# Kernel tuning notes

Hardware: AMD Instinct MI355X
Metric: run time of the kernel (lower is better)

## Reference

```python
import jax, jax.numpy as jnp
import numpy as np

SCALE = 0.2  # scale init arg, clipped to [0,1]


def _relative_corners(rank):
    # [2**rank, rank] matrix of +-1 corner coordinates
    return jnp.array([[float(int(c)) * 2.0 - 1.0 for c in format(i, '0%db' % rank)]
                      for i in range(2 ** rank)], dtype=jnp.float32)


def _affine_from_noise(random_u):
    # random_u: [B, 2**r, r] uniform(0,1) -> random_scale uniform(1-SCALE, 1)
    B, n, r = random_u.shape
    out_c = _relative_corners(r)                                  # [2^r, r]
    random_scale = (1.0 - SCALE) + SCALE * random_u
    src = out_c[None] * random_scale                              # [B, 2^r, r]
    ones_col = jnp.ones((B, n, 1), jnp.float32)
    A = jnp.broadcast_to(
        jnp.concatenate([out_c, jnp.ones((n, 1), jnp.float32)], -1)[None],
        (B, n, r + 1))                                            # output corners (homog.)
    Bmat = jnp.concatenate([src, ones_col], -1)                   # source corners (homog.)
    # least-squares solve A X = B  (matrix_solve_ls): X = (A^T A)^{-1} A^T B
    AtA = jnp.einsum('bni,bnj->bij', A, A)
    AtB = jnp.einsum('bni,bnj->bij', A, Bmat)
    X = jnp.linalg.solve(AtA, AtB)                                # [B, r+1, r+1]
    return jnp.transpose(X, (0, 2, 1))                            # transform, [B, r+1, r+1]


def _make_grid(transform, spatial_shape):
    # AffineGridWarper: output voxel coords normalized to [-1,1], affine-mapped,
    # then converted to source pixel coordinates [0, size-1].
    r = len(spatial_shape)
    axes = [jnp.linspace(-1.0, 1.0, s) for s in spatial_shape]
    mesh = jnp.stack(jnp.meshgrid(*axes, indexing='ij'), -1)      # [D,H,W,r]
    mesh_h = jnp.concatenate(
        [mesh, jnp.ones(tuple(spatial_shape) + (1,), jnp.float32)], -1)
    coords = jnp.einsum('dhwj,bij->bdhwi', mesh_h, transform[:, :r, :])  # [B,D,H,W,r]
    sizes = jnp.array(spatial_shape, jnp.float32)
    return (coords + 1.0) * (sizes - 1.0) * 0.5                   # pixel coords


def _resample_linear_zero(img, coords):
    # trilinear interpolation with zero boundary: out-of-range corners contribute 0
    # img: [B,D,H,W,C], coords: [B,D,H,W,3] (pixel coordinates)
    B = img.shape[0]
    sp = jnp.array(img.shape[1:4], jnp.int32)
    f = jnp.floor(coords)
    frac = coords - f                                             # [B,D,H,W,3]
    i0 = f.astype(jnp.int32)
    bidx = jnp.arange(B)[:, None, None, None]
    out = jnp.zeros(img.shape, img.dtype)
    for corner in range(8):  # fixed structural loop over 2^3 interpolation corners
        off = jnp.array([(corner >> 2) & 1, (corner >> 1) & 1, corner & 1], jnp.int32)
        idx = i0 + off
        valid = jnp.all((idx >= 0) & (idx < sp), axis=-1)         # [B,D,H,W]
        ci = jnp.clip(idx, 0, sp - 1)
        vals = img[bidx, ci[..., 0], ci[..., 1], ci[..., 2]]      # [B,D,H,W,C]
        w = jnp.prod(jnp.where(off == 1, frac, 1.0 - frac), axis=-1)
        w = w * valid.astype(img.dtype)
        out = out + vals * w[..., None]
    return out


def setup_inputs() -> dict:
    key = jax.random.key(0)
    k1, k2 = jax.random.split(key)
    input_tensor = jax.random.normal(k1, (8, 128, 128, 128, 1), dtype=jnp.float32)
    random_u = jax.random.uniform(k2, (8, 8, 3), dtype=jnp.float32)
    return {"input_tensor": input_tensor, "random_u": random_u}


def reference(input_tensor, random_u):
    transform = _affine_from_noise(random_u)                      # [B,4,4]
    grid = _make_grid(transform, input_tensor.shape[1:4])         # [B,D,H,W,3]
    return _resample_linear_zero(input_tensor, grid)
```

## Files before the change

kernel.cpp:

```cpp
#include <hip/hip_runtime.h>

#define NB   8
#define NS   128
#define VOXELS_PER_B (NS*NS*NS)

__global__ void affine_from_noise_kernel(const float* __restrict__ u,
                                         float* __restrict__ T) {
    int b = threadIdx.x;
    if (b >= NB) return;
    float t[3][4];
#pragma unroll
    for (int i = 0; i < 3; ++i)
#pragma unroll
        for (int j = 0; j < 4; ++j) t[i][j] = 0.0f;

#pragma unroll
    for (int n = 0; n < 8; ++n) {
        float c0 = (n & 4) ? 1.0f : -1.0f;
        float c1 = (n & 2) ? 1.0f : -1.0f;
        float c2 = (n & 1) ? 1.0f : -1.0f;
        float c[3] = {c0, c1, c2};
#pragma unroll
        for (int i = 0; i < 3; ++i) {
            float s  = 0.8f + 0.2f * u[(b * 8 + n) * 3 + i];
            float bi = c[i] * s;
            t[i][0] += c[0] * bi;
            t[i][1] += c[1] * bi;
            t[i][2] += c[2] * bi;
            t[i][3] += bi;
        }
    }
#pragma unroll
    for (int i = 0; i < 3; ++i)
#pragma unroll
        for (int j = 0; j < 4; ++j)
            T[b * 12 + i * 4 + j] = t[i][j] * 0.125f;
}

__global__ __launch_bounds__(256) void warp_resample_kernel(
        const float* __restrict__ img, const float* __restrict__ T,
        float* __restrict__ out) {
    int gid   = blockIdx.x * 256 + threadIdx.x;
    int obase = gid << 2;
    int rem   = obase & (VOXELS_PER_B - 1);
    int d     = rem >> 14;
    int h     = (rem >> 7) & (NS - 1);
    int w     = rem & (NS - 1);

    __shared__ float t[12];
    int b = (int)((blockIdx.x * 1024u) >> 21);
    if (threadIdx.x < 12) t[threadIdx.x] = T[b * 12 + threadIdx.x];
    __syncthreads();

    const float inv = 2.0f / 127.0f;
    float x = -1.0f + d * inv;
    float y = -1.0f + h * inv;
    float z = -1.0f + w * inv;

    float q0 = (t[0] * x + t[1] * y + t[2]  * z + t[3]  + 1.0f) * 63.5f;
    float q1 = (t[4] * x + t[5] * y + t[6]  * z + t[7]  + 1.0f) * 63.5f;
    float q2 = (t[8] * x + t[9] * y + t[10] * z + t[11] + 1.0f) * 63.5f;
    float dp0 = t[2], dp1 = t[6], dp2 = t[10];

    const float* __restrict__ base = img + (size_t)b * VOXELS_PER_B;
    float res[4];

#pragma unroll
    for (int k = 0; k < 4; ++k) {
        float f0 = floorf(q0), f1 = floorf(q1), f2 = floorf(q2);
        int   i0 = (int)f0,    i1 = (int)f1,    i2 = (int)f2;
        float r0 = q0 - f0,    r1 = q1 - f1,    r2 = q2 - f2;

        bool ok = ((unsigned)i0 < 127u) && ((unsigned)i1 < 127u) &&
                  ((unsigned)i2 < 127u);
        float acc;
        if (__all(ok)) {
            const float* p = base + (((i0 << 7) + i1) << 7) + i2;
            float v000 = p[0],            v001 = p[1];
            float v010 = p[NS],           v011 = p[NS + 1];
            float v100 = p[NS * NS],      v101 = p[NS * NS + 1];
            float v110 = p[NS * NS + NS], v111 = p[NS * NS + NS + 1];
            float a0 = v000 + r2 * (v001 - v000);
            float a1 = v010 + r2 * (v011 - v010);
            float a2 = v100 + r2 * (v101 - v100);
            float a3 = v110 + r2 * (v111 - v110);
            float b0 = a0 + r1 * (a1 - a0);
            float b1 = a2 + r1 * (a3 - a2);
            acc = b0 + r0 * (b1 - b0);
        } else {
            float wd0 = (i0 >= 0     && i0 < NS)     ? (1.0f - r0) : 0.0f;
            float wd1 = (i0 + 1 >= 0 && i0 + 1 < NS) ? r0          : 0.0f;
            float wh0 = (i1 >= 0     && i1 < NS)     ? (1.0f - r1) : 0.0f;
            float wh1 = (i1 + 1 >= 0 && i1 + 1 < NS) ? r1          : 0.0f;
            float ww0 = (i2 >= 0     && i2 < NS)     ? (1.0f - r2) : 0.0f;
            float ww1 = (i2 + 1 >= 0 && i2 + 1 < NS) ? r2          : 0.0f;

            int cd0 = min(max(i0,     0), NS - 1);
            int cd1 = min(max(i0 + 1, 0), NS - 1);
            int ch0 = min(max(i1,     0), NS - 1);
            int ch1 = min(max(i1 + 1, 0), NS - 1);
            int cw0 = min(max(i2,     0), NS - 1);
            int cw1 = min(max(i2 + 1, 0), NS - 1);

            int r00 = (cd0 * NS + ch0) * NS;
            int r01 = (cd0 * NS + ch1) * NS;
            int r10 = (cd1 * NS + ch0) * NS;
            int r11 = (cd1 * NS + ch1) * NS;

            float v000 = base[r00 + cw0], v001 = base[r00 + cw1];
            float v010 = base[r01 + cw0], v011 = base[r01 + cw1];
            float v100 = base[r10 + cw0], v101 = base[r10 + cw1];
            float v110 = base[r11 + cw0], v111 = base[r11 + cw1];

            acc = v000 * (wd0 * wh0 * ww0)
                + v001 * (wd0 * wh0 * ww1)
                + v010 * (wd0 * wh1 * ww0)
                + v011 * (wd0 * wh1 * ww1)
                + v100 * (wd1 * wh0 * ww0)
                + v101 * (wd1 * wh0 * ww1)
                + v110 * (wd1 * wh1 * ww0)
                + v111 * (wd1 * wh1 * ww1);
        }
        res[k] = acc;
        q0 += dp0; q1 += dp1; q2 += dp2;
    }

    float4 o = make_float4(res[0], res[1], res[2], res[3]);
    *reinterpret_cast<float4*>(out + obase) = o;
}

extern "C" void kernel_launch(void* const* d_in, const int* in_sizes, int n_in,
                              void* d_out, int out_size, void* d_ws, size_t ws_size,
                              hipStream_t stream) {
    const float* img = (const float*)d_in[0];
    const float* u   = (const float*)d_in[1];
    float* out = (float*)d_out;
    float* T   = (float*)d_ws;

    affine_from_noise_kernel<<<1, 64, 0, stream>>>(u, T);

    int total   = NB * VOXELS_PER_B;
    int threads = total / 4;
    int blocks  = threads / 256;
    warp_resample_kernel<<<blocks, 256, 0, stream>>>(img, T, out);
}
```

Baseline: 146.1 us.

## Fuse transform setup into resample kernel and remap threads along depth

Removes the separate affine-setup kernel launch by having each block compute the 12 transform coefficients from the noise tensor in shared memory. Each thread now owns one (h,w) column and four consecutive depth slices rather than four consecutive w voxels, so lanes within a wavefront cover adjacent w and their gathers coalesce. The in-bounds test is hoisted so a single wave-wide __all decides between the fast and the clamped path for all four samples. In exchange the output writes become four scalar strided stores instead of one float4 store, and every block repeats the small transform computation.

```diff
diff --git a/kernel.cpp b/kernel.cpp
--- a/kernel.cpp
+++ b/kernel.cpp
@@ -4,103 +4,92 @@
 #define NS   128
 #define VOXELS_PER_B (NS*NS*NS)
 
-__global__ void affine_from_noise_kernel(const float* __restrict__ u,
-                                         float* __restrict__ T) {
-    int b = threadIdx.x;
-    if (b >= NB) return;
-    float t[3][4];
-#pragma unroll
-    for (int i = 0; i < 3; ++i)
-#pragma unroll
-        for (int j = 0; j < 4; ++j) t[i][j] = 0.0f;
-
-#pragma unroll
-    for (int n = 0; n < 8; ++n) {
-        float c0 = (n & 4) ? 1.0f : -1.0f;
-        float c1 = (n & 2) ? 1.0f : -1.0f;
-        float c2 = (n & 1) ? 1.0f : -1.0f;
-        float c[3] = {c0, c1, c2};
-#pragma unroll
-        for (int i = 0; i < 3; ++i) {
-            float s  = 0.8f + 0.2f * u[(b * 8 + n) * 3 + i];
-            float bi = c[i] * s;
-            t[i][0] += c[0] * bi;
-            t[i][1] += c[1] * bi;
-            t[i][2] += c[2] * bi;
-            t[i][3] += bi;
-        }
-    }
-#pragma unroll
-    for (int i = 0; i < 3; ++i)
-#pragma unroll
-        for (int j = 0; j < 4; ++j)
-            T[b * 12 + i * 4 + j] = t[i][j] * 0.125f;
-}
-
 __global__ __launch_bounds__(256) void warp_resample_kernel(
-        const float* __restrict__ img, const float* __restrict__ T,
+        const float* __restrict__ img, const float* __restrict__ u,
         float* __restrict__ out) {
-    int gid   = blockIdx.x * 256 + threadIdx.x;
-    int obase = gid << 2;
-    int rem   = obase & (VOXELS_PER_B - 1);
-    int d     = rem >> 14;
-    int h     = (rem >> 7) & (NS - 1);
-    int w     = rem & (NS - 1);
+    int tid = threadIdx.x;
+    int gid = blockIdx.x * 256 + tid;
+    int w    = gid & (NS - 1);
+    int h    = (gid >> 7) & (NS - 1);
+    int dblk = (gid >> 14) & 31;
+    int b    = blockIdx.x >> 11;
 
     __shared__ float t[12];
-    int b = (int)((blockIdx.x * 1024u) >> 21);
-    if (threadIdx.x < 12) t[threadIdx.x] = T[b * 12 + threadIdx.x];
+    if (tid < 12) {
+        int i = tid >> 2;
+        int j = tid & 3;
+        float acc = 0.0f;
+#pragma unroll
+        for (int n = 0; n < 8; ++n) {
+            float ci = (n & (4 >> i)) ? 1.0f : -1.0f;
+            float cj = (j < 3) ? ((n & (4 >> j)) ? 1.0f : -1.0f) : 1.0f;
+            float s  = 0.8f + 0.2f * u[(b * 8 + n) * 3 + i];
+            acc += cj * ci * s;
+        }
+        t[tid] = acc * 0.125f;
+    }
     __syncthreads();
 
     const float inv = 2.0f / 127.0f;
-    float x = -1.0f + d * inv;
-    float y = -1.0f + h * inv;
-    float z = -1.0f + w * inv;
+    int   d0 = dblk << 2;
+    float x  = -1.0f + d0 * inv;
+    float y  = -1.0f + h * inv;
+    float z  = -1.0f + w * inv;
 
     float q0 = (t[0] * x + t[1] * y + t[2]  * z + t[3]  + 1.0f) * 63.5f;
     float q1 = (t[4] * x + t[5] * y + t[6]  * z + t[7]  + 1.0f) * 63.5f;
     float q2 = (t[8] * x + t[9] * y + t[10] * z + t[11] + 1.0f) * 63.5f;
-    float dp0 = t[2], dp1 = t[6], dp2 = t[10];
+    float dq0 = t[0], dq1 = t[4], dq2 = t[8];
+
+    int   i0[4], i1[4], i2[4];
+    float r0[4], r1[4], r2[4];
+    bool  allok = true;
+#pragma unroll
+    for (int k = 0; k < 4; ++k) {
+        float f0 = floorf(q0), f1 = floorf(q1), f2 = floorf(q2);
+        i0[k] = (int)f0; i1[k] = (int)f1; i2[k] = (int)f2;
+        r0[k] = q0 - f0; r1[k] = q1 - f1; r2[k] = q2 - f2;
+        allok = allok && ((unsigned)i0[k] < 127u) &&
+                         ((unsigned)i1[k] < 127u) &&
+                         ((unsigned)i2[k] < 127u);
+        q0 += dq0; q1 += dq1; q2 += dq2;
+    }
 
     const float* __restrict__ base = img + (size_t)b * VOXELS_PER_B;
     float res[4];
 
+    if (__all(allok)) {
 #pragma unroll
-    for (int k = 0; k < 4; ++k) {
-        float f0 = floorf(q0), f1 = floorf(q1), f2 = floorf(q2);
-        int   i0 = (int)f0,    i1 = (int)f1,    i2 = (int)f2;
-        float r0 = q0 - f0,    r1 = q1 - f1,    r2 = q2 - f2;
-
-        bool ok = ((unsigned)i0 < 127u) && ((unsigned)i1 < 127u) &&
-                  ((unsigned)i2 < 127u);
-        float acc;
-        if (__all(ok)) {
-            const float* p = base + (((i0 << 7) + i1) << 7) + i2;
+        for (int k = 0; k < 4; ++k) {
+            const float* p = base + (((i0[k] << 7) + i1[k]) << 7) + i2[k];
             float v000 = p[0],            v001 = p[1];
             float v010 = p[NS],           v011 = p[NS + 1];
             float v100 = p[NS * NS],      v101 = p[NS * NS + 1];
             float v110 = p[NS * NS + NS], v111 = p[NS * NS + NS + 1];
-            float a0 = v000 + r2 * (v001 - v000);
-            float a1 = v010 + r2 * (v011 - v010);
-            float a2 = v100 + r2 * (v101 - v100);
-            float a3 = v110 + r2 * (v111 - v110);
-            float b0 = a0 + r1 * (a1 - a0);
-            float b1 = a2 + r1 * (a3 - a2);
-            acc = b0 + r0 * (b1 - b0);
-        } else {
-            float wd0 = (i0 >= 0     && i0 < NS)     ? (1.0f - r0) : 0.0f;
-            float wd1 = (i0 + 1 >= 0 && i0 + 1 < NS) ? r0          : 0.0f;
-            float wh0 = (i1 >= 0     && i1 < NS)     ? (1.0f - r1) : 0.0f;
-            float wh1 = (i1 + 1 >= 0 && i1 + 1 < NS) ? r1          : 0.0f;
-            float ww0 = (i2 >= 0     && i2 < NS)     ? (1.0f - r2) : 0.0f;
-            float ww1 = (i2 + 1 >= 0 && i2 + 1 < NS) ? r2          : 0.0f;
+            float a0 = v000 + r2[k] * (v001 - v000);
+            float a1 = v010 + r2[k] * (v011 - v010);
+            float a2 = v100 + r2[k] * (v101 - v100);
+            float a3 = v110 + r2[k] * (v111 - v110);
+            float b0 = a0 + r1[k] * (a1 - a0);
+            float b1 = a2 + r1[k] * (a3 - a2);
+            res[k] = b0 + r0[k] * (b1 - b0);
+        }
+    } else {
+#pragma unroll
+        for (int k = 0; k < 4; ++k) {
+            float wd0 = (i0[k] >= 0     && i0[k] < NS)     ? (1.0f - r0[k]) : 0.0f;
+            float wd1 = (i0[k] + 1 >= 0 && i0[k] + 1 < NS) ? r0[k]          : 0.0f;
+            float wh0 = (i1[k] >= 0     && i1[k] < NS)     ? (1.0f - r1[k]) : 0.0f;
+            float wh1 = (i1[k] + 1 >= 0 && i1[k] + 1 < NS) ? r1[k]          : 0.0f;
+            float ww0 = (i2[k] >= 0     && i2[k] < NS)     ? (1.0f - r2[k]) : 0.0f;
+            float ww1 = (i2[k] + 1 >= 0 && i2[k] + 1 < NS) ? r2[k]          : 0.0f;
 
-            int cd0 = min(max(i0,     0), NS - 1);
-            int cd1 = min(max(i0 + 1, 0), NS - 1);
-            int ch0 = min(max(i1,     0), NS - 1);
-            int ch1 = min(max(i1 + 1, 0), NS - 1);
-            int cw0 = min(max(i2,     0), NS - 1);
-            int cw1 = min(max(i2 + 1, 0), NS - 1);
+            int cd0 = min(max(i0[k],     0), NS - 1);
+            int cd1 = min(max(i0[k] + 1, 0), NS - 1);
+            int ch0 = min(max(i1[k],     0), NS - 1);
+            int ch1 = min(max(i1[k] + 1, 0), NS - 1);
+            int cw0 = min(max(i2[k],     0), NS - 1);
+            int cw1 = min(max(i2[k] + 1, 0), NS - 1);
 
             int r00 = (cd0 * NS + ch0) * NS;
             int r01 = (cd0 * NS + ch1) * NS;
@@ -112,21 +101,21 @@
             float v100 = base[r10 + cw0], v101 = base[r10 + cw1];
             float v110 = base[r11 + cw0], v111 = base[r11 + cw1];
 
-            acc = v000 * (wd0 * wh0 * ww0)
-                + v001 * (wd0 * wh0 * ww1)
-                + v010 * (wd0 * wh1 * ww0)
-                + v011 * (wd0 * wh1 * ww1)
-                + v100 * (wd1 * wh0 * ww0)
-                + v101 * (wd1 * wh0 * ww1)
-                + v110 * (wd1 * wh1 * ww0)
-                + v111 * (wd1 * wh1 * ww1);
+            res[k] = v000 * (wd0 * wh0 * ww0)
+                   + v001 * (wd0 * wh0 * ww1)
+                   + v010 * (wd0 * wh1 * ww0)
+                   + v011 * (wd0 * wh1 * ww1)
+                   + v100 * (wd1 * wh0 * ww0)
+                   + v101 * (wd1 * wh0 * ww1)
+                   + v110 * (wd1 * wh1 * ww0)
+                   + v111 * (wd1 * wh1 * ww1);
         }
-        res[k] = acc;
-        q0 += dp0; q1 += dp1; q2 += dp2;
     }
 
-    float4 o = make_float4(res[0], res[1], res[2], res[3]);
-    *reinterpret_cast<float4*>(out + obase) = o;
+    int obase = (((b << 7) + d0) << 14) + (h << 7) + w;
+#pragma unroll
+    for (int k = 0; k < 4; ++k)
+        out[obase + (k << 14)] = res[k];
 }
 
 extern "C" void kernel_launch(void* const* d_in, const int* in_sizes, int n_in,
@@ -135,12 +124,9 @@
     const float* img = (const float*)d_in[0];
     const float* u   = (const float*)d_in[1];
     float* out = (float*)d_out;
-    float* T   = (float*)d_ws;
-
-    affine_from_noise_kernel<<<1, 64, 0, stream>>>(u, T);
 
     int total   = NB * VOXELS_PER_B;
     int threads = total / 4;
     int blocks  = threads / 256;
-    warp_resample_kernel<<<blocks, 256, 0, stream>>>(img, T, out);
+    warp_resample_kernel<<<blocks, 256, 0, stream>>>(img, u, out);
 }
```

After: 146.7 us. About the same (+0.5%).
